# Kernel tuning notes

Hardware: AMD Instinct MI355X
Metric: run time of the kernel (lower is better)

## Reference

```python
import jax, jax.numpy as jnp
import numpy as np

# Sampled-neighborhood cascade sizes (src->dst per layer) and edge counts
N0, N1, N2, N3 = 400000, 200000, 100000, 50000
E1, E2, E3 = 500000, 300000, 150000
DIN, DH = 128, 128


def setup_inputs() -> dict:
    key = jax.random.key(0)
    ks = jax.random.split(key, 24)
    inp = {}
    inp['x'] = jax.random.normal(ks[0], (N0, DIN), jnp.float32)
    inp['src1'] = jax.random.randint(ks[1], (E1,), 0, N0, dtype=jnp.int64)
    inp['dst1'] = jax.random.randint(ks[2], (E1,), 0, N1, dtype=jnp.int64)
    inp['src2'] = jax.random.randint(ks[3], (E2,), 0, N1, dtype=jnp.int64)
    inp['dst2'] = jax.random.randint(ks[4], (E2,), 0, N2, dtype=jnp.int64)
    inp['src3'] = jax.random.randint(ks[5], (E3,), 0, N2, dtype=jnp.int64)
    inp['dst3'] = jax.random.randint(ks[6], (E3,), 0, N3, dtype=jnp.int64)
    # SAGEConv params: lin_l (on aggregated neighbors, with bias), lin_r (root, no bias)
    dims = [(DIN, DH), (DH, DH), (DH, DH)]
    for i, (di, do) in enumerate(dims, start=1):
        s = 1.0 / np.sqrt(di)
        inp[f'Wl{i}'] = jax.random.uniform(ks[6 + 4 * i - 3], (di, do), jnp.float32, -s, s)
        inp[f'Wr{i}'] = jax.random.uniform(ks[6 + 4 * i - 2], (di, do), jnp.float32, -s, s)
        inp[f'b{i}'] = jax.random.uniform(ks[6 + 4 * i - 1], (do,), jnp.float32, -s, s)
        inp[f'a{i}'] = jnp.full((do,), 0.25, jnp.float32)  # PReLU per-channel init
    return inp


def _sage_prelu(x_src, n_dst, src, dst, Wl, Wr, b, alpha):
    # mean aggregation over incoming edges (PyG SAGEConv default aggr='mean')
    x_dst = x_src[:n_dst]                                   # [n_dst, d]
    msg = x_src[src]                                        # [E, d] gather
    summed = jax.ops.segment_sum(msg, dst, num_segments=n_dst)
    cnt = jax.ops.segment_sum(jnp.ones(src.shape[0], x_src.dtype), dst,
                              num_segments=n_dst)
    mean = summed / jnp.maximum(cnt, 1.0)[:, None]
    out = mean @ Wl + b + x_dst @ Wr                        # lin_l(aggr) + lin_r(root)
    return jnp.where(out > 0, out, alpha * out)             # per-channel PReLU


def reference(x, src1, dst1, src2, dst2, src3, dst3,
              Wl1, Wr1, b1, a1, Wl2, Wr2, b2, a2, Wl3, Wr3, b3, a3):
    h = _sage_prelu(x, N1, src1, dst1, Wl1, Wr1, b1, a1)
    h = _sage_prelu(h, N2, src2, dst2, Wl2, Wr2, b2, a2)
    h = _sage_prelu(h, N3, src3, dst3, Wl3, Wr3, b3, a3)
    return h  # [N3, DH]
```

## Files before the change

### kernel.cpp

```cpp
#include <hip/hip_runtime.h>


constexpr int cN0 = 400000, cN1 = 200000, cN2 = 100000, cN3 = 50000;
constexpr int cE1 = 500000, cE2 = 300000, cE3 = 150000;
constexpr int cNT = cN1 + cN2 + cN3;
constexpr int cET = cE1 + cE2 + cE3;

#define NDIV_UP(a, b) (((a) + (b) - 1) / (b))

typedef __attribute__((ext_vector_type(8))) short bf16x8;
typedef __attribute__((ext_vector_type(4))) float f32x4;
typedef __attribute__((ext_vector_type(4))) unsigned u32x4;

__device__ __forceinline__ unsigned fbits(float f) {
  return __builtin_bit_cast(unsigned, f);
}
__device__ __forceinline__ float ffrom(unsigned u) {
  return __builtin_bit_cast(float, u);
}
__device__ __forceinline__ unsigned short f2bf(float f) {
  unsigned u = fbits(f);
  unsigned r = u + 0x7FFFu + ((u >> 16) & 1u);
  return (unsigned short)(r >> 16);
}

__global__ void detect_idx64_kernel(const long long* __restrict__ p, int E,
                                    long long nmax, int* __restrict__ flag) {
  int t = threadIdx.x;
  int n = E < 512 ? E : 512;
  int bad = 0;
  for (int i = t; i < n; i += 64) {
    long long v = p[i];
    if (v < 0 || v >= nmax) bad = 1;
  }
  unsigned long long b = __ballot(bad);
  if (t == 0) *flag = (b == 0ull) ? 1 : 0;
}

__device__ __forceinline__ int load_idx(const void* p, int i, int flag) {
  return flag ? (int)((const long long*)p)[i] : ((const int*)p)[i];
}

__global__ void hist3_kernel(const void* __restrict__ d1, const void* __restrict__ d2,
                             const void* __restrict__ d3, const int* __restrict__ flag,
                             int* __restrict__ CNT) {
  int e = blockIdx.x * 256 + threadIdx.x;
  if (e >= cET) return;
  int f = *flag;
  int d;
  if (e < cE1) d = load_idx(d1, e, f);
  else if (e < cE1 + cE2) d = cN1 + load_idx(d2, e - cE1, f);
  else d = cN1 + cN2 + load_idx(d3, e - cE1 - cE2, f);
  atomicAdd(&CNT[d], 1);
}

__global__ __launch_bounds__(256) void scan_reduce(const int* __restrict__ cnt,
                                                   int n, int* __restrict__ bsum) {
  __shared__ int s[256];
  int t = threadIdx.x;
  int base = blockIdx.x * 1024 + t * 4;
  int v = 0;
  if (base + 3 < n) {
    int4 c = *(const int4*)(cnt + base);
    v = c.x + c.y + c.z + c.w;
  } else {
    for (int i = 0; i < 4; ++i)
      if (base + i < n) v += cnt[base + i];
  }
  s[t] = v;
  __syncthreads();
  for (int off = 128; off > 0; off >>= 1) {
    if (t < off) s[t] += s[t + off];
    __syncthreads();
  }
  if (t == 0) bsum[blockIdx.x] = s[0];
}

__global__ __launch_bounds__(256) void scan_bsums(int* __restrict__ bsum, int nb) {
  __shared__ int s[256];
  int t = threadIdx.x;
  int v0 = (2 * t < nb) ? bsum[2 * t] : 0;
  int v1 = (2 * t + 1 < nb) ? bsum[2 * t + 1] : 0;
  int p = v0 + v1;
  s[t] = p;
  __syncthreads();
  for (int off = 1; off < 256; off <<= 1) {
    int x = (t >= off) ? s[t - off] : 0;
    __syncthreads();
    s[t] += x;
    __syncthreads();
  }
  int excl = s[t] - p;
  if (2 * t < nb) bsum[2 * t] = excl;
  if (2 * t + 1 < nb) bsum[2 * t + 1] = excl + v0;
}

__global__ __launch_bounds__(256) void scan_final(const int* __restrict__ cnt,
                                                  int n, const int* __restrict__ bsum,
                                                  int* __restrict__ offs) {
  __shared__ int s[256];
  int t = threadIdx.x;
  int base = blockIdx.x * 1024 + t * 4;
  int v0 = 0, v1 = 0, v2 = 0, v3 = 0;
  if (base + 3 < n) {
    int4 c = *(const int4*)(cnt + base);
    v0 = c.x; v1 = c.y; v2 = c.z; v3 = c.w;
  } else {
    if (base + 0 < n) v0 = cnt[base + 0];
    if (base + 1 < n) v1 = cnt[base + 1];
    if (base + 2 < n) v2 = cnt[base + 2];
  }
  int tsum = v0 + v1 + v2 + v3;
  s[t] = tsum;
  __syncthreads();
  for (int off = 1; off < 256; off <<= 1) {
    int x = (t >= off) ? s[t - off] : 0;
    __syncthreads();
    s[t] += x;
    __syncthreads();
  }
  int excl = s[t] - tsum;
  int o = bsum[blockIdx.x] + excl;
  if (base + 0 < n) offs[base + 0] = o;
  o += v0;
  if (base + 1 < n) offs[base + 1] = o;
  o += v1;
  if (base + 2 < n) offs[base + 2] = o;
  o += v2;
  if (base + 3 < n) offs[base + 3] = o;
}

__global__ void fill3_kernel(const void* __restrict__ s1, const void* __restrict__ d1,
                             const void* __restrict__ s2, const void* __restrict__ d2,
                             const void* __restrict__ s3, const void* __restrict__ d3,
                             const int* __restrict__ flag,
                             int* __restrict__ OFFS, int* __restrict__ EID) {
  int e = blockIdx.x * 256 + threadIdx.x;
  if (e >= cET) return;
  int f = *flag;
  int s, d;
  if (e < cE1) {
    s = load_idx(s1, e, f);
    d = load_idx(d1, e, f);
  } else if (e < cE1 + cE2) {
    int i = e - cE1;
    s = load_idx(s2, i, f);
    d = cN1 + load_idx(d2, i, f);
  } else {
    int i = e - cE1 - cE2;
    s = load_idx(s3, i, f);
    d = cN1 + cN2 + load_idx(d3, i, f);
  }
  int pos = atomicAdd(&OFFS[d], 1);
  EID[pos] = s;
}

__global__ void pack_w3_kernel(const float* __restrict__ Wl1, const float* __restrict__ Wr1,
                               const float* __restrict__ Wl2, const float* __restrict__ Wr2,
                               const float* __restrict__ Wl3, const float* __restrict__ Wr3,
                               unsigned short* __restrict__ wpk) {
  int idx = blockIdx.x * 256 + threadIdx.x;
  if (idx >= 3 * 16384) return;
  int L = idx >> 14;
  int r = idx & 16383;
  const float* Wl = L == 0 ? Wl1 : (L == 1 ? Wl2 : Wl3);
  const float* Wr = L == 0 ? Wr1 : (L == 1 ? Wr2 : Wr3);
  unsigned short* o = wpk + L * 32768;
  int j = r & 7, l = (r >> 3) & 63, cf = (r >> 9) & 7, ks = r >> 12;
  int k = ks * 32 + (l >> 4) * 8 + j;
  int col = cf * 16 + (l & 15);
  o[r] = f2bf(Wl[k * 128 + col]);
  o[16384 + r] = f2bf(Wr[k * 128 + col]);
}

template <bool SRCF32>
__global__ __launch_bounds__(256) void gather_kernel(
    const void* __restrict__ hsrc, const int* __restrict__ OFFS,
    const int* __restrict__ EID, int rowoff,
    unsigned short* __restrict__ meanB, int n) {
  int row = blockIdx.x * 4 + (threadIdx.x >> 6);
  if (row >= n) return;
  int lane = threadIdx.x & 63;
  int gr = rowoff + row;
  int start = gr ? OFFS[gr - 1] : 0;
  int end = OFFS[gr];
  float a0 = 0.f, a1 = 0.f, b0 = 0.f, b1 = 0.f;
  int i = start;
  for (; i + 1 < end; i += 2) {
    int s0 = EID[i], s1 = EID[i + 1];
    if (SRCF32) {
      float2 v0 = *(const float2*)((const float*)hsrc + (size_t)s0 * 128 + lane * 2);
      float2 v1 = *(const float2*)((const float*)hsrc + (size_t)s1 * 128 + lane * 2);
      a0 += v0.x; a1 += v0.y;
      b0 += v1.x; b1 += v1.y;
    } else {
      unsigned u0 = *(const unsigned*)((const unsigned short*)hsrc + (size_t)s0 * 128 + lane * 2);
      unsigned u1 = *(const unsigned*)((const unsigned short*)hsrc + (size_t)s1 * 128 + lane * 2);
      a0 += ffrom(u0 << 16); a1 += ffrom(u0 & 0xFFFF0000u);
      b0 += ffrom(u1 << 16); b1 += ffrom(u1 & 0xFFFF0000u);
    }
  }
  if (i < end) {
    int s0 = EID[i];
    if (SRCF32) {
      float2 v0 = *(const float2*)((const float*)hsrc + (size_t)s0 * 128 + lane * 2);
      a0 += v0.x; a1 += v0.y;
    } else {
      unsigned u0 = *(const unsigned*)((const unsigned short*)hsrc + (size_t)s0 * 128 + lane * 2);
      a0 += ffrom(u0 << 16); a1 += ffrom(u0 & 0xFFFF0000u);
    }
  }
  a0 += b0; a1 += b1;
  float inv = (end > start) ? 1.0f / (float)(end - start) : 0.0f;
  unsigned o = (unsigned)f2bf(a0 * inv) | ((unsigned)f2bf(a1 * inv) << 16);
  *(unsigned*)(meanB + (size_t)row * 128 + lane * 2) = o;
}

template <bool XF32, bool OUTF32>
__global__ __launch_bounds__(256, 2) void gemm_kernel(
    const unsigned short* __restrict__ meanB, const void* __restrict__ xsrc,
    const unsigned short* __restrict__ W,
    const float* __restrict__ bias, const float* __restrict__ alpha,
    void* __restrict__ outp, int n) {
  __shared__ __align__(16) unsigned short wlds[32768];
  const int tid = threadIdx.x;
  const int lane = tid & 63;
  const int wv = tid >> 6;
  const int rbase = blockIdx.x * 128 + wv * 32;
  const int g = lane >> 4;
  const int r16 = lane & 15;

  bf16x8 am[2][4], ax[2][4];
  float4 xr[2][4][2];
#pragma unroll
  for (int t = 0; t < 2; ++t) {
    const int row = rbase + t * 16 + r16;
    const bool ok = row < n;
#pragma unroll
    for (int ks = 0; ks < 4; ++ks) {
      if (ok) {
        am[t][ks] = *(const bf16x8*)(meanB + (size_t)row * 128 + ks * 32 + g * 8);
        if (XF32) {
          const float* xp = (const float*)xsrc + (size_t)row * 128 + ks * 32 + g * 8;
          xr[t][ks][0] = *(const float4*)(xp);
          xr[t][ks][1] = *(const float4*)(xp + 4);
        } else {
          ax[t][ks] = *(const bf16x8*)((const unsigned short*)xsrc +
                                       (size_t)row * 128 + ks * 32 + g * 8);
        }
      } else {
        am[t][ks] = (bf16x8)0;
        if (XF32) {
          xr[t][ks][0] = make_float4(0.f, 0.f, 0.f, 0.f);
          xr[t][ks][1] = make_float4(0.f, 0.f, 0.f, 0.f);
        } else {
          ax[t][ks] = (bf16x8)0;
        }
      }
    }
  }

  {
    const float4* Wg = (const float4*)W;
    float4* Ws = (float4*)wlds;
#pragma unroll
    for (int i = 0; i < 16; ++i)
      Ws[i * 256 + tid] = Wg[i * 256 + tid];
  }
  __syncthreads();

  if (XF32) {
#pragma unroll
    for (int t = 0; t < 2; ++t)
#pragma unroll
      for (int ks = 0; ks < 4; ++ks) {
        const float* xv = (const float*)&xr[t][ks][0];
        u32x4 w;
#pragma unroll
        for (int p = 0; p < 4; ++p)
          w[p] = (unsigned)f2bf(xv[2 * p]) | ((unsigned)f2bf(xv[2 * p + 1]) << 16);
        ax[t][ks] = __builtin_bit_cast(bf16x8, w);
      }
  }

  f32x4 acc[2][8] = {};
#pragma unroll
  for (int ks = 0; ks < 4; ++ks) {
    const unsigned short* wb = wlds + ks * 4096 + lane * 8;
#pragma unroll
    for (int cf = 0; cf < 8; ++cf) {
      const unsigned short* wp = wb + cf * 512;
      bf16x8 wl = *(const bf16x8*)(wp);
      bf16x8 wr = *(const bf16x8*)(wp + 16384);
#pragma unroll
      for (int t = 0; t < 2; ++t) {
        acc[t][cf] = __builtin_amdgcn_mfma_f32_16x16x32_bf16(am[t][ks], wl, acc[t][cf], 0, 0, 0);
        acc[t][cf] = __builtin_amdgcn_mfma_f32_16x16x32_bf16(ax[t][ks], wr, acc[t][cf], 0, 0, 0);
      }
    }
  }

  const int ocol0 = lane & 15;
  const int orow_off = (lane >> 4) * 4;
#pragma unroll
  for (int cf = 0; cf < 8; ++cf) {
    const int ocol = cf * 16 + ocol0;
    const float b = bias[ocol];
    const float a = alpha[ocol];
#pragma unroll
    for (int t = 0; t < 2; ++t) {
      const int orb = rbase + t * 16 + orow_off;
#pragma unroll
      for (int i = 0; i < 4; ++i) {
        const int orow = orb + i;
        if (orow < n) {
          float v = acc[t][cf][i] + b;
          v = v > 0.f ? v : a * v;
          if (OUTF32) {
            ((float*)outp)[(size_t)orow * 128 + ocol] = v;
          } else {
            ((unsigned short*)outp)[(size_t)orow * 128 + ocol] = f2bf(v);
          }
        }
      }
    }
  }
}

extern "C" void kernel_launch(void* const* d_in, const int* in_sizes, int n_in,
                              void* d_out, int out_size, void* d_ws, size_t ws_size,
                              hipStream_t stream) {
  const float* x = (const float*)d_in[0];
  const void* src1 = d_in[1];
  const void* dst1 = d_in[2];
  const void* src2 = d_in[3];
  const void* dst2 = d_in[4];
  const void* src3 = d_in[5];
  const void* dst3 = d_in[6];
  const float* Wl1 = (const float*)d_in[7];
  const float* Wr1 = (const float*)d_in[8];
  const float* b1  = (const float*)d_in[9];
  const float* a1  = (const float*)d_in[10];
  const float* Wl2 = (const float*)d_in[11];
  const float* Wr2 = (const float*)d_in[12];
  const float* b2  = (const float*)d_in[13];
  const float* a2  = (const float*)d_in[14];
  const float* Wl3 = (const float*)d_in[15];
  const float* Wr3 = (const float*)d_in[16];
  const float* b3  = (const float*)d_in[17];
  const float* a3  = (const float*)d_in[18];

  unsigned short* M1 = (unsigned short*)d_ws;
  unsigned short* M2 = M1 + (size_t)cN1 * 128;
  unsigned short* M3 = M2 + (size_t)cN2 * 128;
  int* CNT = (int*)(M3 + (size_t)cN3 * 128);
  int* OFFS = CNT + cNT;
  int* EID = OFFS + cNT;
  int* bsum = EID + cET;
  int* flag = bsum + 1024;
  unsigned short* wpk = (unsigned short*)(flag + 64);

  const int nb = NDIV_UP(cNT, 1024);

  detect_idx64_kernel<<<1, 64, 0, stream>>>((const long long*)src1, cE1,
                                            (long long)cN0, flag);
  pack_w3_kernel<<<192, 256, 0, stream>>>(Wl1, Wr1, Wl2, Wr2, Wl3, Wr3, wpk);
  hipMemsetAsync(CNT, 0, (size_t)cNT * sizeof(int), stream);
  hist3_kernel<<<NDIV_UP(cET, 256), 256, 0, stream>>>(dst1, dst2, dst3, flag, CNT);
  scan_reduce<<<nb, 256, 0, stream>>>(CNT, cNT, bsum);
  scan_bsums<<<1, 256, 0, stream>>>(bsum, nb);
  scan_final<<<nb, 256, 0, stream>>>(CNT, cNT, bsum, OFFS);
  fill3_kernel<<<NDIV_UP(cET, 256), 256, 0, stream>>>(src1, dst1, src2, dst2,
                                                      src3, dst3, flag, OFFS, EID);

  gather_kernel<true><<<NDIV_UP(cN1, 4), 256, 0, stream>>>(
      x, OFFS, EID, 0, M1, cN1);
  gemm_kernel<true, false><<<NDIV_UP(cN1, 128), 256, 0, stream>>>(
      M1, x, wpk, b1, a1, M1, cN1);

  gather_kernel<false><<<NDIV_UP(cN2, 4), 256, 0, stream>>>(
      M1, OFFS, EID, cN1, M2, cN2);
  gemm_kernel<false, false><<<NDIV_UP(cN2, 128), 256, 0, stream>>>(
      M2, M1, wpk + 32768, b2, a2, M2, cN2);

  gather_kernel<false><<<NDIV_UP(cN3, 4), 256, 0, stream>>>(
      M2, OFFS, EID, cN1 + cN2, M3, cN3);
  gemm_kernel<false, true><<<NDIV_UP(cN3, 128), 256, 0, stream>>>(
      M3, M2, wpk + 65536, b3, a3, d_out, cN3);
}
```

Measured before the change: 363.1 us.

## Gather edges per 16-row block with LDS atomics for load balance

```diff
diff --git a/kernel.cpp b/kernel.cpp
--- a/kernel.cpp
+++ b/kernel.cpp
@@ -134,7 +134,7 @@
                              const void* __restrict__ s2, const void* __restrict__ d2,
                              const void* __restrict__ s3, const void* __restrict__ d3,
                              const int* __restrict__ flag,
-                             int* __restrict__ OFFS, int* __restrict__ EID) {
+                             int* __restrict__ OFFS, int2* __restrict__ EIDD) {
   int e = blockIdx.x * 256 + threadIdx.x;
   if (e >= cET) return;
   int f = *flag;
@@ -152,7 +152,7 @@
     d = cN1 + cN2 + load_idx(d3, i, f);
   }
   int pos = atomicAdd(&OFFS[d], 1);
-  EID[pos] = s;
+  EIDD[pos] = make_int2(s, d);
 }
 
 __global__ void pack_w3_kernel(const float* __restrict__ Wl1, const float* __restrict__ Wr1,
@@ -176,44 +176,68 @@
 template <bool SRCF32>
 __global__ __launch_bounds__(256) void gather_kernel(
     const void* __restrict__ hsrc, const int* __restrict__ OFFS,
-    const int* __restrict__ EID, int rowoff,
+    const int2* __restrict__ EIDD, int rowoff,
     unsigned short* __restrict__ meanB, int n) {
-  int row = blockIdx.x * 4 + (threadIdx.x >> 6);
-  if (row >= n) return;
-  int lane = threadIdx.x & 63;
-  int gr = rowoff + row;
-  int start = gr ? OFFS[gr - 1] : 0;
-  int end = OFFS[gr];
-  float a0 = 0.f, a1 = 0.f, b0 = 0.f, b1 = 0.f;
-  int i = start;
-  for (; i + 1 < end; i += 2) {
-    int s0 = EID[i], s1 = EID[i + 1];
+  __shared__ float acc[16][128];
+  __shared__ float ldsInv[16];
+  const int tid = threadIdx.x;
+  const int r0 = blockIdx.x * 16;
+  const int gr0 = rowoff + r0;
+  const int lastrow = min(r0 + 16, n);
+
+#pragma unroll
+  for (int i = 0; i < 8; ++i)
+    ((float*)acc)[tid + i * 256] = 0.f;
+
+  const int estart = (gr0 == 0) ? 0 : OFFS[gr0 - 1];
+  const int eend = OFFS[rowoff + lastrow - 1];
+
+  if (tid < 16) {
+    float inv = 0.f;
+    const int row = r0 + tid;
+    if (row < n) {
+      const int g = rowoff + row;
+      const int s = g ? OFFS[g - 1] : 0;
+      const int e = OFFS[g];
+      inv = (e > s) ? 1.0f / (float)(e - s) : 0.0f;
+    }
+    ldsInv[tid] = inv;
+  }
+  __syncthreads();
+
+  const int wv = tid >> 6;
+  const int lane = tid & 63;
+  for (int e = estart + wv; e < eend; e += 4) {
+    const int2 sd = EIDD[e];
+    const int r = sd.y - gr0;
+    float v0, v1;
     if (SRCF32) {
-      float2 v0 = *(const float2*)((const float*)hsrc + (size_t)s0 * 128 + lane * 2);
-      float2 v1 = *(const float2*)((const float*)hsrc + (size_t)s1 * 128 + lane * 2);
-      a0 += v0.x; a1 += v0.y;
-      b0 += v1.x; b1 += v1.y;
+      const float* rp = (const float*)hsrc + (size_t)sd.x * 128;
+      v0 = rp[lane];
+      v1 = rp[lane + 64];
     } else {
-      unsigned u0 = *(const unsigned*)((const unsigned short*)hsrc + (size_t)s0 * 128 + lane * 2);
-      unsigned u1 = *(const unsigned*)((const unsigned short*)hsrc + (size_t)s1 * 128 + lane * 2);
-      a0 += ffrom(u0 << 16); a1 += ffrom(u0 & 0xFFFF0000u);
-      b0 += ffrom(u1 << 16); b1 += ffrom(u1 & 0xFFFF0000u);
+      const unsigned short* rp = (const unsigned short*)hsrc + (size_t)sd.x * 128;
+      v0 = ffrom((unsigned)rp[lane] << 16);
+      v1 = ffrom((unsigned)rp[lane + 64] << 16);
     }
-  }
-  if (i < end) {
-    int s0 = EID[i];
-    if (SRCF32) {
-      float2 v0 = *(const float2*)((const float*)hsrc + (size_t)s0 * 128 + lane * 2);
-      a0 += v0.x; a1 += v0.y;
-    } else {
-      unsigned u0 = *(const unsigned*)((const unsigned short*)hsrc + (size_t)s0 * 128 + lane * 2);
-      a0 += ffrom(u0 << 16); a1 += ffrom(u0 & 0xFFFF0000u);
-    }
-  }
-  a0 += b0; a1 += b1;
-  float inv = (end > start) ? 1.0f / (float)(end - start) : 0.0f;
-  unsigned o = (unsigned)f2bf(a0 * inv) | ((unsigned)f2bf(a1 * inv) << 16);
-  *(unsigned*)(meanB + (size_t)row * 128 + lane * 2) = o;
+    atomicAdd(&acc[r][lane], v0);
+    atomicAdd(&acc[r][lane + 64], v1);
+  }
+  __syncthreads();
+
+  const int lr = tid >> 4;
+  const int row = r0 + lr;
+  if (row < n) {
+    const int col = (tid & 15) * 8;
+    const float inv = ldsInv[lr];
+    const float* ap = &acc[lr][col];
+    u32x4 o;
+#pragma unroll
+    for (int p = 0; p < 4; ++p)
+      o[p] = (unsigned)f2bf(ap[2 * p] * inv) |
+             ((unsigned)f2bf(ap[2 * p + 1] * inv) << 16);
+    *(u32x4*)(meanB + (size_t)row * 128 + col) = o;
+  }
 }
 
 template <bool XF32, bool OUTF32>
@@ -355,8 +379,8 @@
   unsigned short* M3 = M2 + (size_t)cN2 * 128;
   int* CNT = (int*)(M3 + (size_t)cN3 * 128);
   int* OFFS = CNT + cNT;
-  int* EID = OFFS + cNT;
-  int* bsum = EID + cET;
+  int2* EIDD = (int2*)(OFFS + cNT);
+  int* bsum = (int*)(EIDD + cET);
   int* flag = bsum + 1024;
   unsigned short* wpk = (unsigned short*)(flag + 64);
 
@@ -371,20 +395,20 @@
   scan_bsums<<<1, 256, 0, stream>>>(bsum, nb);
   scan_final<<<nb, 256, 0, stream>>>(CNT, cNT, bsum, OFFS);
   fill3_kernel<<<NDIV_UP(cET, 256), 256, 0, stream>>>(src1, dst1, src2, dst2,
-                                                      src3, dst3, flag, OFFS, EID);
-
-  gather_kernel<true><<<NDIV_UP(cN1, 4), 256, 0, stream>>>(
-      x, OFFS, EID, 0, M1, cN1);
+                                                      src3, dst3, flag, OFFS, EIDD);
+
+  gather_kernel<true><<<NDIV_UP(cN1, 16), 256, 0, stream>>>(
+      x, OFFS, EIDD, 0, M1, cN1);
   gemm_kernel<true, false><<<NDIV_UP(cN1, 128), 256, 0, stream>>>(
       M1, x, wpk, b1, a1, M1, cN1);
 
-  gather_kernel<false><<<NDIV_UP(cN2, 4), 256, 0, stream>>>(
-      M1, OFFS, EID, cN1, M2, cN2);
+  gather_kernel<false><<<NDIV_UP(cN2, 16), 256, 0, stream>>>(
+      M1, OFFS, EIDD, cN1, M2, cN2);
   gemm_kernel<false, false><<<NDIV_UP(cN2, 128), 256, 0, stream>>>(
       M2, M1, wpk + 32768, b2, a2, M2, cN2);
 
-  gather_kernel<false><<<NDIV_UP(cN3, 4), 256, 0, stream>>>(
-      M2, OFFS, EID, cN1 + cN2, M3, cN3);
+  gather_kernel<false><<<NDIV_UP(cN3, 16), 256, 0, stream>>>(
+      M2, OFFS, EIDD, cN1 + cN2, M3, cN3);
   gemm_kernel<false, true><<<NDIV_UP(cN3, 128), 256, 0, stream>>>(
       M3, M2, wpk + 65536, b3, a3, d_out, cN3);
 }
```

Result: slower. 897.2 us (+147.1%).
